# Optimization experiments

Hardware: AMD Instinct MI355X
Metric: run time of the kernel (lower is better)

## Reference

```python
import jax, jax.numpy as jnp
import numpy as np

HIDDEN = 1024
N_HEADS = 16
HEAD_DIM = HIDDEN // N_HEADS
LN_EPS = 1e-5


def setup_inputs() -> dict:
    key = jax.random.key(0)
    ks = jax.random.split(key, 8)
    B, S = 4, 1024
    inp = {
        'input_tensor': jax.random.normal(ks[0], (B, S, HIDDEN), dtype=jnp.float32),
        'memory_tensor': jax.random.normal(ks[1], (B, S, HIDDEN), dtype=jnp.float32),
        'attention_mask': jnp.ones((B, S, S), dtype=jnp.float32),
        'wq': jax.random.normal(ks[2], (HIDDEN, HIDDEN), dtype=jnp.float32) * 0.02,
        'wk': jax.random.normal(ks[3], (HIDDEN, HIDDEN), dtype=jnp.float32) * 0.02,
        'wv': jax.random.normal(ks[4], (HIDDEN, HIDDEN), dtype=jnp.float32) * 0.02,
        'wo': jax.random.normal(ks[5], (HIDDEN, HIDDEN), dtype=jnp.float32) * 0.02,
        'ln_gamma': jnp.ones((HIDDEN,), dtype=jnp.float32),
        'ln_beta': jnp.zeros((HIDDEN,), dtype=jnp.float32),
        'seq_length': 1024,
        'enc_seq_length': 1024,
    }
    return inp


def _layernorm(x, gamma, beta):
    mu = jnp.mean(x, axis=-1, keepdims=True)
    var = jnp.mean(jnp.square(x - mu), axis=-1, keepdims=True)
    return (x - mu) * jax.lax.rsqrt(var + LN_EPS) * gamma + beta


def reference(input_tensor, memory_tensor, attention_mask, wq, wk, wv, wo,
              ln_gamma, ln_beta, seq_length, enc_seq_length):
    B = input_tensor.shape[0]
    S = seq_length
    x2d = input_tensor.reshape(-1, HIDDEN)            # [B*S, H]
    normed = _layernorm(x2d, ln_gamma, ln_beta)       # LayerPreprocess
    # is_encdec_att=False: memory = normed output (memory_tensor unused)
    mem = normed
    # torch nn.Linear(bias=False): y = x @ W.T
    q = (normed @ wq.T).reshape(B, S, N_HEADS, HEAD_DIM).transpose(0, 2, 1, 3)
    k = (mem @ wk.T).reshape(B, S, N_HEADS, HEAD_DIM).transpose(0, 2, 1, 3)
    v = (mem @ wv.T).reshape(B, S, N_HEADS, HEAD_DIM).transpose(0, 2, 1, 3)
    scale = 1.0 / np.sqrt(float(HEAD_DIM))
    scores = jnp.einsum('bhqd,bhkd->bhqk', q, k) * scale   # [B, H, S, S]
    scores = scores - 10000.0 * (1.0 - attention_mask[:, None, :, :])
    probs = jax.nn.softmax(scores, axis=-1)
    ctx = jnp.einsum('bhqk,bhkd->bhqd', probs, v)          # [B, H, S, dh]
    ctx = ctx.transpose(0, 2, 1, 3).reshape(B * S, HIDDEN)
    attn_out = ctx @ wo.T
    # LayerPostprocess (dropout=0): residual add with raw (pre-LN) input
    return attn_out + x2d
```

## Files before the change

### kernel.cpp

```cpp
#include <hip/hip_runtime.h>
#include <hip/hip_bf16.h>


typedef unsigned short u16;
typedef __attribute__((ext_vector_type(8))) short short8;
typedef __attribute__((ext_vector_type(4))) float f32x4;

__device__ __forceinline__ u16 f2bf(float f) {
  union { float f; unsigned u; } cv; cv.f = f;
  unsigned u = cv.u + 0x7fffu + ((cv.u >> 16) & 1u);
  return (u16)(u >> 16);
}

__device__ __forceinline__ void gload_lds16(const void* g, void* l) {
  __builtin_amdgcn_global_load_lds(
      (const __attribute__((address_space(1))) void*)g,
      (__attribute__((address_space(3))) void*)l, 16, 0, 0);
}

__device__ __forceinline__ f32x4 mfma16(short8 a, short8 b, f32x4 c) {
  return __builtin_amdgcn_mfma_f32_16x16x32_bf16(a, b, c, 0, 0, 0);
}

__global__ __launch_bounds__(256) void ln_kernel(const float* __restrict__ x,
                                                 const float* __restrict__ gamma,
                                                 const float* __restrict__ beta,
                                                 u16* __restrict__ outn) {
  __shared__ float sm[4];
  const int row = blockIdx.x, t = threadIdx.x;
  float4 v = ((const float4*)(x + (size_t)row * 1024))[t];
  float s = v.x + v.y + v.z + v.w;
#pragma unroll
  for (int off = 32; off; off >>= 1) s += __shfl_down(s, off);
  if ((t & 63) == 0) sm[t >> 6] = s;
  __syncthreads();
  const float mu = (sm[0] + sm[1] + sm[2] + sm[3]) * (1.0f / 1024.0f);
  const float dx = v.x - mu, dy = v.y - mu, dz = v.z - mu, dw = v.w - mu;
  float vs = dx * dx + dy * dy + dz * dz + dw * dw;
  __syncthreads();
#pragma unroll
  for (int off = 32; off; off >>= 1) vs += __shfl_down(vs, off);
  if ((t & 63) == 0) sm[t >> 6] = vs;
  __syncthreads();
  const float var = (sm[0] + sm[1] + sm[2] + sm[3]) * (1.0f / 1024.0f);
  const float rstd = rsqrtf(var + 1e-5f);
  float4 g = ((const float4*)gamma)[t];
  float4 b = ((const float4*)beta)[t];
  uint2 pk;
  pk.x = (unsigned)f2bf(dx * rstd * g.x + b.x) | ((unsigned)f2bf(dy * rstd * g.y + b.y) << 16);
  pk.y = (unsigned)f2bf(dz * rstd * g.z + b.z) | ((unsigned)f2bf(dw * rstd * g.w + b.w) << 16);
  *(uint2*)&outn[(size_t)row * 1024 + t * 4] = pk;
}

__global__ __launch_bounds__(256) void cvt_w(const float* __restrict__ wq,
                                             const float* __restrict__ wk,
                                             const float* __restrict__ wv,
                                             const float* __restrict__ wo,
                                             u16* __restrict__ out) {
  const int i = blockIdx.x * 256 + threadIdx.x;
  const int e = i * 4;
  const int seg = e >> 20;
  const int off = e & 1048575;
  const float* src = (seg == 0) ? wq : (seg == 1) ? wk : (seg == 2) ? wv : wo;
  float4 v = *(const float4*)(src + off);
  uint2 pk;
  pk.x = (unsigned)f2bf(v.x) | ((unsigned)f2bf(v.y) << 16);
  pk.y = (unsigned)f2bf(v.z) | ((unsigned)f2bf(v.w) << 16);
  *(uint2*)&out[e] = pk;
}

template <int MODE>
__global__ __launch_bounds__(256) void gemm_bt(const u16* __restrict__ A,
                                               const u16* __restrict__ Bm,
                                               u16* __restrict__ outQ, u16* __restrict__ outK,
                                               u16* __restrict__ outVt,
                                               float* __restrict__ outF,
                                               const float* __restrict__ resid) {
  constexpr int BM = (MODE == 0) ? 128 : 64;
  constexpr int MI = BM / 32;
  constexpr int ASZ = BM * 32;
  constexpr int BSZ = 128 * 32;
  constexpr int STG = 2 * ASZ + 2 * BSZ;
  constexpr int SMEM = (MODE == 0) ? (STG > 18432 ? STG : 18432) : STG;
  __shared__ u16 sm[SMEM];

  const int m0 = blockIdx.y * BM, n0 = blockIdx.x * 128;
  const int t = threadIdx.x;
  const int wid = t >> 6, lane = t & 63;
  const int wm = (wid >> 1) * (BM / 2), wn = (wid & 1) * 64;
  const int lr = lane & 15, lg = lane >> 4;
  const int swz = (lg ^ ((lr >> 1) & 3)) << 3;
  f32x4 acc[MI][4] = {};

  const int scol = (((t & 3) ^ ((t >> 3) & 3)) << 3);
  const u16* aT = A + (size_t)(m0 + (t >> 2)) * 1024 + scol;
  const u16* bT = Bm + (size_t)(n0 + (t >> 2)) * 1024 + scol;

  auto STAGE = [&](int buf, int kt) {
    const int k0 = kt * 32;
#pragma unroll
    for (int cc = 0; cc < BM / 64; cc++)
      gload_lds16(aT + (size_t)cc * 65536 + k0, &sm[buf * ASZ + cc * 2048 + t * 8]);
#pragma unroll
    for (int cc = 0; cc < 2; cc++)
      gload_lds16(bT + (size_t)cc * 65536 + k0, &sm[2 * ASZ + buf * BSZ + cc * 2048 + t * 8]);
  };

  STAGE(0, 0);
  asm volatile("s_waitcnt vmcnt(0)" ::: "memory");
  __builtin_amdgcn_s_barrier();
  __builtin_amdgcn_sched_barrier(0);

  int cur = 0;
  for (int kt = 0; kt < 32; kt++) {
    STAGE(cur ^ 1, (kt + 1) & 31);

    short8 af[MI], bfr[4];
#pragma unroll
    for (int mi = 0; mi < MI; mi++)
      af[mi] = *(const short8*)&sm[cur * ASZ + (wm + mi * 16 + lr) * 32 + swz];
#pragma unroll
    for (int ni = 0; ni < 4; ni++)
      bfr[ni] = *(const short8*)&sm[2 * ASZ + cur * BSZ + (wn + ni * 16 + lr) * 32 + swz];
    __builtin_amdgcn_s_setprio(1);
#pragma unroll
    for (int mi = 0; mi < MI; mi++)
#pragma unroll
      for (int ni = 0; ni < 4; ni++)
        acc[mi][ni] = mfma16(af[mi], bfr[ni], acc[mi][ni]);
    __builtin_amdgcn_s_setprio(0);

    asm volatile("s_waitcnt vmcnt(0)" ::: "memory");
    __builtin_amdgcn_s_barrier();
    __builtin_amdgcn_sched_barrier(0);
    cur ^= 1;
  }

  if (MODE == 1) {
#pragma unroll
    for (int mi = 0; mi < MI; mi++)
#pragma unroll
      for (int ni = 0; ni < 4; ni++)
#pragma unroll
        for (int r = 0; r < 4; r++) {
          const int i = m0 + wm + mi * 16 + lg * 4 + r;
          const int j = n0 + wn + ni * 16 + lr;
          const size_t o = (size_t)i * 1024 + j;
          outF[o] = acc[mi][ni][r] + resid[o];
        }
    return;
  }

  const int seg = (n0 + wn) >> 10;
  const int g8 = lane >> 3, j8 = lane & 7;
  if (seg < 2) {
    u16* epi = &sm[wid * 4608];
    const float qs = (seg == 0) ? 0.125f : 1.0f;
#pragma unroll
    for (int mi = 0; mi < 4; mi++)
#pragma unroll
      for (int ni = 0; ni < 4; ni++)
#pragma unroll
        for (int r = 0; r < 4; r++)
          epi[(mi * 16 + lg * 4 + r) * 72 + ni * 16 + lr] = f2bf(acc[mi][ni][r] * qs);
    __syncthreads();
    u16* dst = (seg == 0) ? outQ : outK;
    const int h = ((n0 + wn) & 1023) >> 6;
#pragma unroll
    for (int it = 0; it < 8; it++) {
      const int ml = it * 8 + g8;
      short8 v = *(const short8*)&epi[ml * 72 + j8 * 8];
      const int i = m0 + wm + ml;
      const int b = i >> 10, s_ = i & 1023;
      *(short8*)&dst[((size_t)(b * 16 + h) * 1024 + s_) * 64 + j8 * 8] = v;
    }
  } else {
    u16* epi = &sm[wid * 4096];
#pragma unroll
    for (int mi = 0; mi < 4; mi++)
#pragma unroll
      for (int ni = 0; ni < 4; ni++) {
        const int n = ni * 16 + lr;
        const int c2 = 4 * mi + lg;
        uint2 w;
        w.x = (unsigned)f2bf(acc[mi][ni][0]) | ((unsigned)f2bf(acc[mi][ni][1]) << 16);
        w.y = (unsigned)f2bf(acc[mi][ni][2]) | ((unsigned)f2bf(acc[mi][ni][3]) << 16);
        *(uint2*)&epi[n * 64 + ((c2 ^ (n & 15)) << 2)] = w;
      }
    __syncthreads();
    const int h = ((n0 + wn) & 1023) >> 6;
    const int b = (m0 + wm) >> 10, sb = (m0 + wm) & 1023;
#pragma unroll
    for (int it = 0; it < 8; it++) {
      const int n = it * 8 + g8;
      uint2 w0 = *(const uint2*)&epi[n * 64 + (((2 * j8) ^ (n & 15)) << 2)];
      uint2 w1 = *(const uint2*)&epi[n * 64 + (((2 * j8 + 1) ^ (n & 15)) << 2)];
      uint4 w; w.x = w0.x; w.y = w0.y; w.z = w1.x; w.w = w1.y;
      *(uint4*)&outVt[((size_t)(b * 16 + h) * 64 + n) * 1024 + sb + j8 * 8] = w;
    }
  }
}

__global__ __launch_bounds__(256) void flash_kernel(const u16* __restrict__ Qg,
                                                    const u16* __restrict__ Kg,
                                                    const u16* __restrict__ Vt,
                                                    const float* __restrict__ mask,
                                                    u16* __restrict__ ctx) {
  const int h = blockIdx.x, qt = blockIdx.y, b = blockIdx.z;
  const int bh = b * 16 + h;
  __shared__ u16 Ks[2][4096];
  __shared__ u16 Vs[2][4096];
  __shared__ u16 Ps[4][1024];
  const int t = threadIdx.x, wid = t >> 6, lane = t & 63;
  const int lr = lane & 15, lg = lane >> 4;
  const int hR = lr & 7;
  const int qbase = qt * 64 + wid * 16;

  short8 qf0, qf1;
  {
    const u16* qrow = Qg + ((size_t)bh * 1024 + qbase + lr) * 64;
    qf0 = *(const short8*)(qrow + lg * 8);
    qf1 = *(const short8*)(qrow + 32 + lg * 8);
  }
  f32x4 octx[4] = {};
  float m_ln = -1e30f, l_ln = 0.0f;

  const u16* kS0 = Kg + (size_t)bh * 65536;
  const u16* vS0 = Vt + (size_t)bh * 65536;
  const int srow = t >> 3, scb = t & 7;

  const float* mptr = mask + ((size_t)b * 1024 + qbase + lr) * 1024 + lg * 4;

  auto STAGE = [&](int nb, int kt) {
#pragma unroll
    for (int c = 0; c < 2; c++) {
      const int row = c * 32 + srow;
      const int sc = (scb ^ (row & 7)) * 8;
      gload_lds16(kS0 + (size_t)(kt * 64 + row) * 64 + sc, &Ks[nb][c * 2048 + t * 8]);
      gload_lds16(vS0 + (size_t)row * 1024 + kt * 64 + sc, &Vs[nb][c * 2048 + t * 8]);
    }
  };

  STAGE(0, 0);
  float mc[4][4];
#pragma unroll
  for (int kn = 0; kn < 4; kn++) {
    float4 v = *(const float4*)(mptr + kn * 16);
    mc[kn][0] = v.x; mc[kn][1] = v.y; mc[kn][2] = v.z; mc[kn][3] = v.w;
  }
  asm volatile("s_waitcnt vmcnt(0)" ::: "memory");
  __builtin_amdgcn_s_barrier();
  __builtin_amdgcn_sched_barrier(0);

  int cur = 0;
  for (int kt = 0; kt < 16; kt++) {
    const int ktn = (kt < 15) ? kt + 1 : 15;
    STAGE(cur ^ 1, ktn);
    float mnx[4][4];
#pragma unroll
    for (int kn = 0; kn < 4; kn++) {
      float4 v = *(const float4*)(mptr + ktn * 64 + kn * 16);
      mnx[kn][0] = v.x; mnx[kn][1] = v.y; mnx[kn][2] = v.z; mnx[kn][3] = v.w;
    }

    float sv[4][4];
#pragma unroll
    for (int kn = 0; kn < 4; kn++) {
      const int R = kn * 16 + lr;
      short8 kf0 = *(const short8*)&Ks[cur][R * 64 + ((lg ^ hR) << 3)];
      short8 kf1 = *(const short8*)&Ks[cur][R * 64 + (((lg + 4) ^ hR) << 3)];
      f32x4 s = {};
      s = mfma16(kf0, qf0, s);
      s = mfma16(kf1, qf1, s);
      __builtin_amdgcn_s_setprio(0);
#pragma unroll
      for (int r = 0; r < 4; r++)
        sv[kn][r] = s[r] + fmaf(10000.f, mc[kn][r], -10000.f);
    }

    float mx0 = fmaxf(fmaxf(sv[0][0], sv[0][1]), fmaxf(sv[0][2], sv[0][3]));
    float mx1 = fmaxf(fmaxf(sv[1][0], sv[1][1]), fmaxf(sv[1][2], sv[1][3]));
    float mx2 = fmaxf(fmaxf(sv[2][0], sv[2][1]), fmaxf(sv[2][2], sv[2][3]));
    float mx3 = fmaxf(fmaxf(sv[3][0], sv[3][1]), fmaxf(sv[3][2], sv[3][3]));
    float mt = fmaxf(fmaxf(mx0, mx1), fmaxf(mx2, mx3));
    mt = fmaxf(mt, __shfl_xor(mt, 16));
    mt = fmaxf(mt, __shfl_xor(mt, 32));
    const float mn = fmaxf(m_ln, mt);
    const float f = __expf(m_ln - mn);
    m_ln = mn;
    float ps = 0.0f;
#pragma unroll
    for (int kn = 0; kn < 4; kn++) {
      float p0 = __expf(sv[kn][0] - mn), p1 = __expf(sv[kn][1] - mn);
      float p2 = __expf(sv[kn][2] - mn), p3 = __expf(sv[kn][3] - mn);
      sv[kn][0] = p0; sv[kn][1] = p1; sv[kn][2] = p2; sv[kn][3] = p3;
      ps += (p0 + p1) + (p2 + p3);
    }
    ps += __shfl_xor(ps, 16);
    ps += __shfl_xor(ps, 32);
    l_ln = l_ln * f + ps;

    float fb[4];
#pragma unroll
    for (int r = 0; r < 4; r++)
      fb[r] = __shfl(f, (lane & 48) | (lg * 4 + r), 64);
#pragma unroll
    for (int g = 0; g < 4; g++)
#pragma unroll
      for (int r = 0; r < 4; r++) octx[g][r] *= fb[r];

    const int pswz = (lr & 7) << 1;
#pragma unroll
    for (int kn = 0; kn < 4; kn++) {
      uint2 w;
      w.x = (unsigned)f2bf(sv[kn][0]) | ((unsigned)f2bf(sv[kn][1]) << 16);
      w.y = (unsigned)f2bf(sv[kn][2]) | ((unsigned)f2bf(sv[kn][3]) << 16);
      *(uint2*)&Ps[wid][lr * 64 + (((kn * 4 + lg) ^ pswz) << 2)] = w;
    }
    short8 pa0 = *(const short8*)&Ps[wid][lr * 64 + (((2 * lg) ^ pswz) << 2)];
    short8 pa1 = *(const short8*)&Ps[wid][lr * 64 + (((8 + 2 * lg) ^ pswz) << 2)];

    __builtin_amdgcn_s_setprio(1);
#pragma unroll
    for (int g = 0; g < 4; g++) {
      const int R = g * 16 + lr;
      short8 vf0 = *(const short8*)&Vs[cur][R * 64 + ((lg ^ hR) << 3)];
      short8 vf1 = *(const short8*)&Vs[cur][R * 64 + (((lg + 4) ^ hR) << 3)];
      octx[g] = mfma16(pa0, vf0, octx[g]);
      octx[g] = mfma16(pa1, vf1, octx[g]);
    }
    __builtin_amdgcn_s_setprio(0);

    asm volatile("s_waitcnt vmcnt(0)" ::: "memory");
    __builtin_amdgcn_s_barrier();
    __builtin_amdgcn_sched_barrier(0);
    cur ^= 1;
#pragma unroll
    for (int kn = 0; kn < 4; kn++)
#pragma unroll
      for (int r = 0; r < 4; r++) mc[kn][r] = mnx[kn][r];
  }

  float lb[4];
#pragma unroll
  for (int r = 0; r < 4; r++)
    lb[r] = __shfl(l_ln, (lane & 48) | (lg * 4 + r), 64);
#pragma unroll
  for (int g = 0; g < 4; g++)
#pragma unroll
    for (int r = 0; r < 4; r++) {
      const int qr = qbase + lg * 4 + r;
      ctx[((size_t)b * 1024 + qr) * 1024 + h * 64 + g * 16 + lr] = f2bf(octx[g][r] / lb[r]);
    }
}

extern "C" void kernel_launch(void* const* d_in, const int* in_sizes, int n_in,
                              void* d_out, int out_size, void* d_ws, size_t ws_size,
                              hipStream_t stream) {
  const float* x     = (const float*)d_in[0];
  const float* mask  = (const float*)d_in[2];
  const float* wq    = (const float*)d_in[3];
  const float* wk    = (const float*)d_in[4];
  const float* wv    = (const float*)d_in[5];
  const float* wo    = (const float*)d_in[6];
  const float* gamma = (const float*)d_in[7];
  const float* beta  = (const float*)d_in[8];
  float* out = (float*)d_out;

  char* ws = (char*)d_ws;
  u16* normed = (u16*)(ws);
  u16* wcat   = (u16*)(ws + (8ull << 20));
  u16* Qg     = (u16*)(ws + (16ull << 20));
  u16* Kg     = (u16*)(ws + (24ull << 20));
  u16* Vtg    = (u16*)(ws + (32ull << 20));
  u16* ctx    = (u16*)(ws + (40ull << 20));
  u16* wo_bf  = wcat + 3072ull * 1024;

  ln_kernel<<<4096, 256, 0, stream>>>(x, gamma, beta, normed);
  cvt_w<<<4096, 256, 0, stream>>>(wq, wk, wv, wo, wcat);
  gemm_bt<0><<<dim3(24, 32), 256, 0, stream>>>(normed, wcat, Qg, Kg, Vtg, nullptr, nullptr);
  flash_kernel<<<dim3(16, 16, 4), 256, 0, stream>>>(Qg, Kg, Vtg, mask, ctx);
  gemm_bt<1><<<dim3(8, 64), 256, 0, stream>>>(ctx, wo_bf, nullptr, nullptr, nullptr, out, x);
}
```

Baseline: 223.3 us.

## Triple-buffer GEMM loads, lazy softmax rescale, exp2 scaling, remap flash blocks

The GEMM moves from double to triple buffering, issuing loads two k-steps ahead with partial vmcnt waits so a single barrier per iteration covers the memory latency. The flash kernel folds log2(e) into the Q scale and the mask constant so it can use exp2f. It skips rescaling the output accumulator unless the running max grows by more than 8, remaps the 1D grid so blocks are ordered differently across XCDs, and unrolls the key loop by two. Hardware packed bf16 conversion replaces the manual rounding. The lazy rescale lets unnormalized exponentials grow up to 2^8, which could affect precision, and the extra LDS buffer may reduce GEMM occupancy.

```diff
diff --git a/kernel.cpp b/kernel.cpp
--- a/kernel.cpp
+++ b/kernel.cpp
@@ -10,6 +10,12 @@
   union { float f; unsigned u; } cv; cv.f = f;
   unsigned u = cv.u + 0x7fffu + ((cv.u >> 16) & 1u);
   return (u16)(u >> 16);
+}
+
+__device__ __forceinline__ unsigned pk_bf16(float lo, float hi) {
+  unsigned r;
+  asm("v_cvt_pk_bf16_f32 %0, %1, %2" : "=v"(r) : "v"(lo), "v"(hi));
+  return r;
 }
 
 __device__ __forceinline__ void gload_lds16(const void* g, void* l) {
@@ -80,9 +86,7 @@
   constexpr int MI = BM / 32;
   constexpr int ASZ = BM * 32;
   constexpr int BSZ = 128 * 32;
-  constexpr int STG = 2 * ASZ + 2 * BSZ;
-  constexpr int SMEM = (MODE == 0) ? (STG > 18432 ? STG : 18432) : STG;
-  __shared__ u16 sm[SMEM];
+  __shared__ u16 sm[3 * (ASZ + BSZ)];
 
   const int m0 = blockIdx.y * BM, n0 = blockIdx.x * 128;
   const int t = threadIdx.x;
@@ -103,25 +107,30 @@
       gload_lds16(aT + (size_t)cc * 65536 + k0, &sm[buf * ASZ + cc * 2048 + t * 8]);
 #pragma unroll
     for (int cc = 0; cc < 2; cc++)
-      gload_lds16(bT + (size_t)cc * 65536 + k0, &sm[2 * ASZ + buf * BSZ + cc * 2048 + t * 8]);
+      gload_lds16(bT + (size_t)cc * 65536 + k0, &sm[3 * ASZ + buf * BSZ + cc * 2048 + t * 8]);
   };
 
   STAGE(0, 0);
-  asm volatile("s_waitcnt vmcnt(0)" ::: "memory");
-  __builtin_amdgcn_s_barrier();
-  __builtin_amdgcn_sched_barrier(0);
-
-  int cur = 0;
+  STAGE(1, 1);
+
+  int cb = 0, sb = 2;
   for (int kt = 0; kt < 32; kt++) {
-    STAGE(cur ^ 1, (kt + 1) & 31);
+    if constexpr (MODE == 0)
+      asm volatile("s_waitcnt vmcnt(4)" ::: "memory");
+    else
+      asm volatile("s_waitcnt vmcnt(3)" ::: "memory");
+    __builtin_amdgcn_s_barrier();
+    __builtin_amdgcn_sched_barrier(0);
+
+    STAGE(sb, (kt + 2) & 31);
 
     short8 af[MI], bfr[4];
 #pragma unroll
     for (int mi = 0; mi < MI; mi++)
-      af[mi] = *(const short8*)&sm[cur * ASZ + (wm + mi * 16 + lr) * 32 + swz];
+      af[mi] = *(const short8*)&sm[cb * ASZ + (wm + mi * 16 + lr) * 32 + swz];
 #pragma unroll
     for (int ni = 0; ni < 4; ni++)
-      bfr[ni] = *(const short8*)&sm[2 * ASZ + cur * BSZ + (wn + ni * 16 + lr) * 32 + swz];
+      bfr[ni] = *(const short8*)&sm[3 * ASZ + cb * BSZ + (wn + ni * 16 + lr) * 32 + swz];
     __builtin_amdgcn_s_setprio(1);
 #pragma unroll
     for (int mi = 0; mi < MI; mi++)
@@ -130,10 +139,10 @@
         acc[mi][ni] = mfma16(af[mi], bfr[ni], acc[mi][ni]);
     __builtin_amdgcn_s_setprio(0);
 
-    asm volatile("s_waitcnt vmcnt(0)" ::: "memory");
-    __builtin_amdgcn_s_barrier();
-    __builtin_amdgcn_sched_barrier(0);
-    cur ^= 1;
+    const int nb = cb;
+    cb = (cb == 2) ? 0 : cb + 1;
+    sb = (sb == 2) ? 0 : sb + 1;
+    (void)nb;
   }
 
   if (MODE == 1) {
@@ -151,11 +160,14 @@
     return;
   }
 
+  asm volatile("s_waitcnt vmcnt(0)" ::: "memory");
+  __syncthreads();
+
   const int seg = (n0 + wn) >> 10;
   const int g8 = lane >> 3, j8 = lane & 7;
   if (seg < 2) {
     u16* epi = &sm[wid * 4608];
-    const float qs = (seg == 0) ? 0.125f : 1.0f;
+    const float qs = (seg == 0) ? 0.18033688f : 1.0f;
 #pragma unroll
     for (int mi = 0; mi < 4; mi++)
 #pragma unroll
@@ -183,20 +195,20 @@
         const int n = ni * 16 + lr;
         const int c2 = 4 * mi + lg;
         uint2 w;
-        w.x = (unsigned)f2bf(acc[mi][ni][0]) | ((unsigned)f2bf(acc[mi][ni][1]) << 16);
-        w.y = (unsigned)f2bf(acc[mi][ni][2]) | ((unsigned)f2bf(acc[mi][ni][3]) << 16);
+        w.x = pk_bf16(acc[mi][ni][0], acc[mi][ni][1]);
+        w.y = pk_bf16(acc[mi][ni][2], acc[mi][ni][3]);
         *(uint2*)&epi[n * 64 + ((c2 ^ (n & 15)) << 2)] = w;
       }
     __syncthreads();
     const int h = ((n0 + wn) & 1023) >> 6;
-    const int b = (m0 + wm) >> 10, sb = (m0 + wm) & 1023;
+    const int b = (m0 + wm) >> 10, sbm = (m0 + wm) & 1023;
 #pragma unroll
     for (int it = 0; it < 8; it++) {
       const int n = it * 8 + g8;
       uint2 w0 = *(const uint2*)&epi[n * 64 + (((2 * j8) ^ (n & 15)) << 2)];
       uint2 w1 = *(const uint2*)&epi[n * 64 + (((2 * j8 + 1) ^ (n & 15)) << 2)];
       uint4 w; w.x = w0.x; w.y = w0.y; w.z = w1.x; w.w = w1.y;
-      *(uint4*)&outVt[((size_t)(b * 16 + h) * 64 + n) * 1024 + sb + j8 * 8] = w;
+      *(uint4*)&outVt[((size_t)(b * 16 + h) * 64 + n) * 1024 + sbm + j8 * 8] = w;
     }
   }
 }
@@ -206,7 +218,9 @@
                                                     const u16* __restrict__ Vt,
                                                     const float* __restrict__ mask,
                                                     u16* __restrict__ ctx) {
-  const int h = blockIdx.x, qt = blockIdx.y, b = blockIdx.z;
+  const int id = blockIdx.x;
+  const int nid = (id & 7) * 128 + (id >> 3);
+  const int qt = nid & 15, h = (nid >> 4) & 15, b = nid >> 8;
   const int bh = b * 16 + h;
   __shared__ u16 Ks[2][4096];
   __shared__ u16 Vs[2][4096];
@@ -253,6 +267,7 @@
   __builtin_amdgcn_sched_barrier(0);
 
   int cur = 0;
+#pragma unroll 2
   for (int kt = 0; kt < 16; kt++) {
     const int ktn = (kt < 15) ? kt + 1 : 15;
     STAGE(cur ^ 1, ktn);
@@ -272,49 +287,51 @@
       f32x4 s = {};
       s = mfma16(kf0, qf0, s);
       s = mfma16(kf1, qf1, s);
-      __builtin_amdgcn_s_setprio(0);
 #pragma unroll
       for (int r = 0; r < 4; r++)
-        sv[kn][r] = s[r] + fmaf(10000.f, mc[kn][r], -10000.f);
-    }
-
-    float mx0 = fmaxf(fmaxf(sv[0][0], sv[0][1]), fmaxf(sv[0][2], sv[0][3]));
-    float mx1 = fmaxf(fmaxf(sv[1][0], sv[1][1]), fmaxf(sv[1][2], sv[1][3]));
-    float mx2 = fmaxf(fmaxf(sv[2][0], sv[2][1]), fmaxf(sv[2][2], sv[2][3]));
-    float mx3 = fmaxf(fmaxf(sv[3][0], sv[3][1]), fmaxf(sv[3][2], sv[3][3]));
-    float mt = fmaxf(fmaxf(mx0, mx1), fmaxf(mx2, mx3));
+        sv[kn][r] = s[r] + fmaf(14426.9504f, mc[kn][r], -14426.9504f);
+    }
+
+    float mt = fmaxf(fmaxf(fmaxf(sv[0][0], sv[0][1]), fmaxf(sv[0][2], sv[0][3])),
+                     fmaxf(fmaxf(sv[1][0], sv[1][1]), fmaxf(sv[1][2], sv[1][3])));
+    mt = fmaxf(mt, fmaxf(fmaxf(fmaxf(sv[2][0], sv[2][1]), fmaxf(sv[2][2], sv[2][3])),
+                         fmaxf(fmaxf(sv[3][0], sv[3][1]), fmaxf(sv[3][2], sv[3][3]))));
     mt = fmaxf(mt, __shfl_xor(mt, 16));
     mt = fmaxf(mt, __shfl_xor(mt, 32));
-    const float mn = fmaxf(m_ln, mt);
-    const float f = __expf(m_ln - mn);
-    m_ln = mn;
+    if (__any(mt > m_ln + 8.0f)) {
+      const float mn = fmaxf(m_ln, mt);
+      const float f = exp2f(m_ln - mn);
+      m_ln = mn;
+      l_ln *= f;
+      float fb[4];
+#pragma unroll
+      for (int r = 0; r < 4; r++)
+        fb[r] = __shfl(f, (lane & 48) | (lg * 4 + r), 64);
+#pragma unroll
+      for (int g = 0; g < 4; g++)
+#pragma unroll
+        for (int r = 0; r < 4; r++) octx[g][r] *= fb[r];
+    }
+
     float ps = 0.0f;
 #pragma unroll
     for (int kn = 0; kn < 4; kn++) {
-      float p0 = __expf(sv[kn][0] - mn), p1 = __expf(sv[kn][1] - mn);
-      float p2 = __expf(sv[kn][2] - mn), p3 = __expf(sv[kn][3] - mn);
-      sv[kn][0] = p0; sv[kn][1] = p1; sv[kn][2] = p2; sv[kn][3] = p3;
-      ps += (p0 + p1) + (p2 + p3);
+      sv[kn][0] = exp2f(sv[kn][0] - m_ln);
+      sv[kn][1] = exp2f(sv[kn][1] - m_ln);
+      sv[kn][2] = exp2f(sv[kn][2] - m_ln);
+      sv[kn][3] = exp2f(sv[kn][3] - m_ln);
+      ps += (sv[kn][0] + sv[kn][1]) + (sv[kn][2] + sv[kn][3]);
     }
     ps += __shfl_xor(ps, 16);
     ps += __shfl_xor(ps, 32);
-    l_ln = l_ln * f + ps;
-
-    float fb[4];
-#pragma unroll
-    for (int r = 0; r < 4; r++)
-      fb[r] = __shfl(f, (lane & 48) | (lg * 4 + r), 64);
-#pragma unroll
-    for (int g = 0; g < 4; g++)
-#pragma unroll
-      for (int r = 0; r < 4; r++) octx[g][r] *= fb[r];
+    l_ln += ps;
 
     const int pswz = (lr & 7) << 1;
 #pragma unroll
     for (int kn = 0; kn < 4; kn++) {
       uint2 w;
-      w.x = (unsigned)f2bf(sv[kn][0]) | ((unsigned)f2bf(sv[kn][1]) << 16);
-      w.y = (unsigned)f2bf(sv[kn][2]) | ((unsigned)f2bf(sv[kn][3]) << 16);
+      w.x = pk_bf16(sv[kn][0], sv[kn][1]);
+      w.y = pk_bf16(sv[kn][2], sv[kn][3]);
       *(uint2*)&Ps[wid][lr * 64 + (((kn * 4 + lg) ^ pswz) << 2)] = w;
     }
     short8 pa0 = *(const short8*)&Ps[wid][lr * 64 + (((2 * lg) ^ pswz) << 2)];
@@ -379,6 +396,6 @@
   ln_kernel<<<4096, 256, 0, stream>>>(x, gamma, beta, normed);
   cvt_w<<<4096, 256, 0, stream>>>(wq, wk, wv, wo, wcat);
   gemm_bt<0><<<dim3(24, 32), 256, 0, stream>>>(normed, wcat, Qg, Kg, Vtg, nullptr, nullptr);
-  flash_kernel<<<dim3(16, 16, 4), 256, 0, stream>>>(Qg, Kg, Vtg, mask, ctx);
+  flash_kernel<<<1024, 256, 0, stream>>>(Qg, Kg, Vtg, mask, ctx);
   gemm_bt<1><<<dim3(8, 64), 256, 0, stream>>>(ctx, wo_bf, nullptr, nullptr, nullptr, out, x);
 }
```

Result: slower. 237.5 us (+6.4%).
